# Kernel optimization log

Hardware: AMD Instinct MI355X
Metric: run time of the kernel (lower is better)

Reference implementation:

```python
import jax, jax.numpy as jnp
import numpy as np

N = 100000      # nodes
F_IN = 500      # num_features
H = 128         # num_hidden
C = 40          # num_classes
E = 3200000     # structural edges
K = 5           # knn neighbors


def setup_inputs() -> dict:
    key = jax.random.key(0)
    ks = jax.random.split(key, 9)
    x = jax.random.normal(ks[0], (N, F_IN), dtype=jnp.float32)
    edge_index = jax.random.randint(ks[1], (2, E), 0, N, dtype=jnp.int64)
    # knn graph: source i repeated K times, targets random (stand-in for cosine-KNN)
    src = jnp.repeat(jnp.arange(N, dtype=jnp.int64), K)
    dst = jax.random.randint(ks[2], (K * N,), 0, N, dtype=jnp.int64)
    edge_index_knn = jnp.stack([src, dst])
    s = lambda f: np.float32(1.0 / np.sqrt(f))
    W1 = jax.random.normal(ks[3], (F_IN, H), jnp.float32) * s(F_IN)
    b1 = jnp.zeros((H,), jnp.float32)
    W2 = jax.random.normal(ks[4], (2 * H, C), jnp.float32) * s(2 * H)
    b2 = jnp.zeros((C,), jnp.float32)
    Wlin = jax.random.normal(ks[5], (C, 2 * C), jnp.float32) * s(2 * C)  # torch Linear layout [out,in]
    blin = jnp.zeros((C,), jnp.float32)
    return {"x": x, "edge_index": edge_index, "edge_index_knn": edge_index_knn,
            "W1": W1, "b1": b1, "W2": W2, "b2": b2, "Wlin": Wlin, "blin": blin}


def gcn_conv(x, W, b, edge_index):
    # PyG GCNConv: add self-loops, symmetric normalization deg^-1/2 A deg^-1/2, x@W, scatter-add, +bias
    n = x.shape[0]
    loop = jnp.arange(n, dtype=edge_index.dtype)
    row = jnp.concatenate([edge_index[0], loop])  # sources (gathered)
    col = jnp.concatenate([edge_index[1], loop])  # targets (scattered)
    deg = jax.ops.segment_sum(jnp.ones_like(col, x.dtype), col, num_segments=n)
    dinv = jnp.where(deg > 0, jax.lax.rsqrt(jnp.maximum(deg, 1e-12)), 0.0).astype(x.dtype)
    norm = dinv[row] * dinv[col]                      # [E+n]
    h = x @ W                                          # [n, out]
    agg = jax.ops.segment_sum(h[row] * norm[:, None], col, num_segments=n)
    return agg + b


def reference(x, edge_index, edge_index_knn, W1, b1, W2, b2, Wlin, blin):
    h1 = gcn_conv(x, W1, b1, edge_index)
    h1_2 = gcn_conv(x, W1, b1, edge_index_knn)
    R1 = jax.nn.relu(jnp.concatenate([h1, h1_2], axis=1))  # dropout identity (eval mode)
    h2 = gcn_conv(R1, W2, b2, edge_index)
    h2_2 = gcn_conv(R1, W2, b2, edge_index_knn)
    R2 = jnp.concatenate([h2, h2_2], axis=1)
    logits = R2 @ Wlin.T + blin
    return jax.nn.log_softmax(logits, axis=1)
```

## Files before the change

kernel.cpp:

```cpp
#include <hip/hip_runtime.h>
#include <stdint.h>

#define NN   100000
#define FIN  500
#define HID  128
#define KP1  512
#define K2   256
#define CO   40
#define NPQ  80
#define NBUCK 391
#define CAPB_S 9216
#define CAPB_K 1536

typedef __attribute__((ext_vector_type(8))) short short8;
typedef __attribute__((ext_vector_type(4))) float float4v;
typedef __attribute__((address_space(3))) unsigned int as3_u32;
typedef __attribute__((address_space(1))) unsigned int as1_u32;

__device__ __forceinline__ unsigned short f2bf(float f) {
  unsigned u = __float_as_uint(f);
  u = u + 0x7fffu + ((u >> 16) & 1u);
  return (unsigned short)(u >> 16);
}
__device__ __forceinline__ float bf2f(unsigned short s) {
  return __uint_as_float(((unsigned)s) << 16);
}
__device__ __forceinline__ void gl_lds16(const void* g, void* l) {
  __builtin_amdgcn_global_load_lds((const as1_u32*)g, (as3_u32*)l, 16, 0, 0);
}

__global__ __launch_bounds__(256) void k_bin(
    const int* __restrict__ ei, int nS, int nb1S, int* __restrict__ gcur_s, int* __restrict__ gbin_s,
    const int* __restrict__ eik, int nK, int* __restrict__ gcur_k, int* __restrict__ gbin_k) {
  __shared__ int cnt[NBUCK];
  __shared__ int base[NBUCK];
  const int b = blockIdx.x;
  const bool knn = (b >= nb1S);
  const int* src = knn ? eik      : ei;
  const int* tgt = knn ? eik + nK : ei + nS;
  const int n    = knn ? nK : nS;
  int* gcur      = knn ? gcur_k : gcur_s;
  int* gbin      = knn ? gbin_k : gbin_s;
  const int capb = knn ? CAPB_K : CAPB_S;
  const int ebase = (knn ? b - nb1S : b) * 4096;
  const int t = threadIdx.x;

  for (int i = t; i < NBUCK; i += 256) cnt[i] = 0;
  __syncthreads();
  int s[16], g[16];
#pragma unroll
  for (int i = 0; i < 16; ++i) {
    const int e = ebase + i * 256 + t;
    const bool v = e < n;
    s[i] = v ? src[e] : 0;
    g[i] = v ? tgt[e] : -1;
    if (v) atomicAdd(&cnt[g[i] >> 8], 1);
  }
  __syncthreads();
  for (int i = t; i < NBUCK; i += 256) {
    const int c = cnt[i];
    base[i] = c ? atomicAdd(&gcur[i], c) : 0;
    cnt[i] = 0;
  }
  __syncthreads();
#pragma unroll
  for (int i = 0; i < 16; ++i) {
    if (g[i] >= 0) {
      const int bkt = g[i] >> 8;
      const int pos = base[bkt] + atomicAdd(&cnt[bkt], 1);
      if (pos < capb) gbin[bkt * capb + pos] = (s[i] << 8) | (g[i] & 255);
    }
  }
}

__global__ __launch_bounds__(512) void k_bscan(const int* __restrict__ gcur_s, int* __restrict__ bscan_s,
                                               const int* __restrict__ gcur_k, int* __restrict__ bscan_k) {
  __shared__ int sd[512];
  const int* gcur = blockIdx.x ? gcur_k : gcur_s;
  int* bscan      = blockIdx.x ? bscan_k : bscan_s;
  const int t = threadIdx.x;
  const int v = (t < NBUCK) ? gcur[t] : 0;
  sd[t] = v;
  __syncthreads();
  for (int off = 1; off < 512; off <<= 1) {
    const int x = (t >= off) ? sd[t - off] : 0;
    __syncthreads(); sd[t] += x; __syncthreads();
  }
  if (t < NBUCK) bscan[t] = sd[t] - v;
}

__global__ __launch_bounds__(256) void k_csr(
    const int* __restrict__ gcur_s, const int* __restrict__ gbin_s, const int* __restrict__ bscan_s,
    int* __restrict__ rp_s, int2* __restrict__ colw_s, float* __restrict__ dinv_s,
    const int* __restrict__ gcur_k, const int* __restrict__ gbin_k, const int* __restrict__ bscan_k,
    int* __restrict__ rp_k, int2* __restrict__ colw_k, float* __restrict__ dinv_k) {
  __shared__ int cnt[256];
  __shared__ int base[256];
  const int b0 = blockIdx.x;
  const bool knn = (b0 >= NBUCK);
  const int b = knn ? b0 - NBUCK : b0;
  const int* gcur  = knn ? gcur_k  : gcur_s;
  const int* gbin  = knn ? gbin_k  : gbin_s;
  const int* bscan = knn ? bscan_k : bscan_s;
  int* rp     = knn ? rp_k   : rp_s;
  int2* colw  = knn ? colw_k : colw_s;
  float* dinv = knn ? dinv_k : dinv_s;
  const int capb = knn ? CAPB_K : CAPB_S;
  const int t = threadIdx.x;
  int nB = gcur[b]; if (nB > capb) nB = capb;
  const int gb0 = b * capb;
  const int gbase = bscan[b];

  cnt[t] = 0;
  __syncthreads();
  for (int i = t; i < nB; i += 256) atomicAdd(&cnt[gbin[gb0 + i] & 255], 1);
  __syncthreads();
  const int myc = cnt[t];
  base[t] = myc;
  __syncthreads();
  for (int off = 1; off < 256; off <<= 1) {
    const int x = (t >= off) ? base[t - off] : 0;
    __syncthreads(); base[t] += x; __syncthreads();
  }
  const int excl = base[t] - myc;
  const int tg = b * 256 + t;
  if (tg < NN) { rp[tg] = gbase + excl; dinv[tg] = rsqrtf((float)(myc + 1)); }
  if (tg == NN) rp[NN] = gbase + excl;
  __syncthreads();
  base[t] = excl; cnt[t] = 0;
  __syncthreads();
  for (int i = t; i < nB; i += 256) {
    const int e = gbin[gb0 + i];
    const int tl = e & 255;
    const int pos = atomicAdd(&cnt[tl], 1);
    colw[gbase + base[tl] + pos] = make_int2(e >> 8, 0);
  }
}

__global__ __launch_bounds__(256) void k_fuse(
    int2* __restrict__ colw_s, const float* __restrict__ dinv_s, int nS, int nbF,
    int2* __restrict__ colw_k, const float* __restrict__ dinv_k, int nK) {
  const int b = blockIdx.x;
  if (b < nbF) {
    const int i = b * 256 + threadIdx.x;
    if (i < nS) {
      const int s = colw_s[i].x;
      colw_s[i].y = __float_as_int(dinv_s[s]);
    }
  } else {
    const int i = (b - nbF) * 256 + threadIdx.x;
    if (i < nK) {
      const int s = colw_k[i].x;
      colw_k[i].y = __float_as_int(dinv_k[s]);
    }
  }
}

__global__ void k_w1t(const float* __restrict__ W1, unsigned short* __restrict__ W1T) {
  int idx = blockIdx.x * 256 + threadIdx.x;
  int n = idx >> 9, k = idx & 511;
  float v = (k < FIN) ? W1[k * HID + n] : 0.f;
  W1T[idx] = f2bf(v);
}
__global__ void k_wpq(const float* __restrict__ W2, const float* __restrict__ Wl,
                      const float* __restrict__ b2, const float* __restrict__ bl,
                      unsigned short* __restrict__ WpqT, float* __restrict__ cb) {
  const int idx = blockIdx.x * 256 + threadIdx.x;
  const int n = idx >> 8, k = idx & 255;
  const int o = (n < CO) ? n : n - CO;
  const int joff = (n < CO) ? 0 : CO;
  float s = 0.f;
#pragma unroll 8
  for (int j = 0; j < CO; ++j) s += W2[k * CO + j] * Wl[o * NPQ + joff + j];
  WpqT[n * K2 + k] = f2bf(s);
  if (blockIdx.x == 0 && threadIdx.x < CO) {
    const int oo = threadIdx.x;
    float c = bl[oo];
    for (int j = 0; j < CO; ++j) c += b2[j] * (Wl[oo * NPQ + j] + Wl[oo * NPQ + CO + j]);
    cb[oo] = c;
  }
}

__global__ __launch_bounds__(256) void k_gemm1(const float* __restrict__ x,
    const unsigned short* __restrict__ W1T, const float* __restrict__ zbuf,
    unsigned short* __restrict__ H1b) {
  __shared__ float Als[2][512 * 4];
  __shared__ unsigned short Bls[2][512 * 8];
  const int t = threadIdx.x;
  const int wv = t >> 6, lane = t & 63;
  const int qd = lane >> 4, mr = lane & 15;
  const int m0 = blockIdx.x * 64;

  float4v acc[8];
  const float4v zf4 = {0.f, 0.f, 0.f, 0.f};
#pragma unroll
  for (int b = 0; b < 8; ++b) acc[b] = zf4;

  auto stage = [&](int kk, int pb) {
    const int k0 = kk * 32;
#pragma unroll
    for (int i = 0; i < 2; ++i) {
      const int cb = i * 256 + wv * 64;
      const int q = cb + lane;
      const int kg = q >> 6, m = q & 63;
      const int gm = m0 + m, kb = k0 + kg * 4;
      const float* gp = (gm < NN && kb < FIN) ? (x + (size_t)gm * FIN + kb) : zbuf;
      gl_lds16(gp, &Als[pb][cb * 4]);
    }
#pragma unroll
    for (int i = 0; i < 2; ++i) {
      const int cb = i * 256 + wv * 64;
      const int q = cb + lane;
      const int kg = q >> 7, n = q & 127;
      gl_lds16(W1T + n * KP1 + k0 + kg * 8, &Bls[pb][cb * 8]);
    }
  };

  stage(0, 0);
  for (int kk = 0; kk < 16; ++kk) {
    const int cur = kk & 1;
    if (kk + 1 < 16) {
      stage(kk + 1, cur ^ 1);
      asm volatile("s_waitcnt vmcnt(4)" ::: "memory");
    } else {
      asm volatile("s_waitcnt vmcnt(0)" ::: "memory");
    }
    __builtin_amdgcn_s_barrier();

    short8 af;
    {
      const int m = wv * 16 + mr;
      const float4v a0 = *(const float4v*)&Als[cur][((2 * qd) * 64 + m) * 4];
      const float4v a1 = *(const float4v*)&Als[cur][((2 * qd + 1) * 64 + m) * 4];
      af[0] = (short)f2bf(a0[0]); af[1] = (short)f2bf(a0[1]);
      af[2] = (short)f2bf(a0[2]); af[3] = (short)f2bf(a0[3]);
      af[4] = (short)f2bf(a1[0]); af[5] = (short)f2bf(a1[1]);
      af[6] = (short)f2bf(a1[2]); af[7] = (short)f2bf(a1[3]);
    }
#pragma unroll
    for (int ct = 0; ct < 8; ++ct) {
      const short8 bf = *(const short8*)&Bls[cur][(qd * 128 + ct * 16 + mr) * 8];
      acc[ct] = __builtin_amdgcn_mfma_f32_16x16x32_bf16(af, bf, acc[ct], 0, 0, 0);
    }
    __builtin_amdgcn_s_barrier();
  }

  const int rb = m0 + wv * 16 + qd * 4;
#pragma unroll
  for (int ct = 0; ct < 8; ++ct) {
    const int col = ct * 16 + mr;
#pragma unroll
    for (int j = 0; j < 4; ++j) {
      const int r = rb + j;
      if (r < NN) H1b[(size_t)r * HID + col] = f2bf(acc[ct][j]);
    }
  }
}

__global__ __launch_bounds__(256) void k_gemm2(const unsigned short* __restrict__ R1b,
    const unsigned short* __restrict__ WpqT, const unsigned short* __restrict__ zbuf,
    unsigned short* __restrict__ PQ) {
  __shared__ unsigned short Als[512 * 8];
  __shared__ unsigned short Bls[320 * 8];
  const int t = threadIdx.x;
  const int wv = t >> 6, lane = t & 63;
  const int qd = lane >> 4, mr = lane & 15;
  const int m0 = blockIdx.x * 128;

  float4v acc[2][5];
  const float4v zf4 = {0.f, 0.f, 0.f, 0.f};
#pragma unroll
  for (int a = 0; a < 2; ++a)
#pragma unroll
    for (int b = 0; b < 5; ++b) acc[a][b] = zf4;

  for (int kk = 0; kk < 8; ++kk) {
    const int k0 = kk * 32;
    __syncthreads();
#pragma unroll
    for (int i = 0; i < 2; ++i) {
      const int cb = (wv * 2 + i) * 64;
      const int q = cb + lane;
      const int kg = q >> 7, m = q & 127;
      const int gm = m0 + m;
      const unsigned short* gp = (gm < NN) ? (R1b + (size_t)gm * K2 + k0 + kg * 8) : zbuf;
      gl_lds16(gp, &Als[cb * 8]);
    }
    {
      const int cb = wv * 64;
      const int q = cb + lane;
      const int kg = q / 80, n = q % 80;
      gl_lds16(WpqT + n * K2 + k0 + kg * 8, &Bls[cb * 8]);
      if (wv == 0) {
        const int cb2 = 4 * 64;
        const int q2 = cb2 + lane;
        const int kg2 = q2 / 80, n2 = q2 % 80;
        gl_lds16(WpqT + n2 * K2 + k0 + kg2 * 8, &Bls[cb2 * 8]);
      }
    }
    __syncthreads();
    short8 af[2];
#pragma unroll
    for (int rt = 0; rt < 2; ++rt)
      af[rt] = *(const short8*)&Als[(qd * 128 + wv * 32 + rt * 16 + mr) * 8];
#pragma unroll
    for (int ct = 0; ct < 5; ++ct) {
      const short8 bf = *(const short8*)&Bls[(qd * 80 + ct * 16 + mr) * 8];
      acc[0][ct] = __builtin_amdgcn_mfma_f32_16x16x32_bf16(af[0], bf, acc[0][ct], 0, 0, 0);
      acc[1][ct] = __builtin_amdgcn_mfma_f32_16x16x32_bf16(af[1], bf, acc[1][ct], 0, 0, 0);
    }
  }
#pragma unroll
  for (int rt = 0; rt < 2; ++rt) {
    const int rb = m0 + wv * 32 + rt * 16 + qd * 4;
#pragma unroll
    for (int ct = 0; ct < 5; ++ct) {
      const int col = ct * 16 + mr;
#pragma unroll
      for (int j = 0; j < 4; ++j) {
        const int r = rb + j;
        if (r < NN) PQ[(size_t)r * NPQ + col] = f2bf(acc[rt][ct][j]);
      }
    }
  }
}

__device__ __forceinline__ void ld8(const int2* __restrict__ cw, int base, int e1, bool full,
                                    int2* __restrict__ q) {
  if (full) {
#pragma unroll
    for (int j = 0; j < 8; ++j) q[j] = cw[base + j];
  } else {
    const int e1c = e1 - 1;
#pragma unroll
    for (int j = 0; j < 8; ++j) {
      const int ee = base + j;
      int2 t = cw[(ee < e1) ? ee : e1c];
      t.y = (ee < e1) ? t.y : 0;
      q[j] = t;
    }
  }
}
__device__ __forceinline__ void g8(const int2* __restrict__ q,
    const unsigned* __restrict__ H32, int lane, unsigned* __restrict__ d) {
#pragma unroll
  for (int j = 0; j < 8; ++j) d[j] = H32[(size_t)q[j].x * 64 + lane];
}
__device__ __forceinline__ void f8(const int2* __restrict__ q, const unsigned* __restrict__ d,
                                   float& ax, float& ay) {
#pragma unroll
  for (int j = 0; j < 8; ++j) {
    const float w = __int_as_float(q[j].y);
    ax += w * __uint_as_float(d[j] << 16);
    ay += w * __uint_as_float(d[j] & 0xffff0000u);
  }
}

__global__ __launch_bounds__(256) void k_agg1(
    const int* __restrict__ rp_s, const int2* __restrict__ colw_s, const float* __restrict__ dinv_s,
    const int* __restrict__ rp_k, const int2* __restrict__ colw_k, const float* __restrict__ dinv_k,
    const unsigned short* __restrict__ H, const float* __restrict__ bias,
    unsigned short* __restrict__ out) {
  const int wv = threadIdx.x >> 6, lane = threadIdx.x & 63;
  const int c = blockIdx.x * 4 + wv;
  if (c >= NN) return;
  const unsigned* H32 = (const unsigned*)H;
  const int e0s = __builtin_amdgcn_readfirstlane(rp_s[c]);
  const int e1s = __builtin_amdgcn_readfirstlane(rp_s[c + 1]);
  const int e0k = __builtin_amdgcn_readfirstlane(rp_k[c]);
  const int e1k = __builtin_amdgcn_readfirstlane(rp_k[c + 1]);
  const int nbS = (e1s - e0s + 7) >> 3;
  const int nbK = (e1k - e0k + 7) >> 3;

  int2 q0[8], q1[8], qk[8];
  unsigned d0[8], d1[8], dk[8];
  const unsigned pc = H32[(size_t)c * 64 + lane];
  if (nbS > 0) { ld8(colw_s, e0s, e1s, e0s + 8 <= e1s, q0); g8(q0, H32, lane, d0); }
  if (nbS > 1) { ld8(colw_s, e0s + 8, e1s, e0s + 16 <= e1s, q1); g8(q1, H32, lane, d1); }
  if (nbK > 0) { ld8(colw_k, e0k, e1k, e0k + 8 <= e1k, qk); g8(qk, H32, lane, dk); }

  const float dcs = dinv_s[c], dck = dinv_k[c];
  const float slo = __uint_as_float(pc << 16);
  const float shi = __uint_as_float(pc & 0xffff0000u);
  float ax = dcs * slo, ay = dcs * shi;
  float bx = dck * slo, by = dck * shi;

  int b = 0;
  while (b + 2 < nbS) {
    f8(q0, d0, ax, ay);
    {
      const int bs = e0s + (b + 2) * 8;
      ld8(colw_s, bs, e1s, bs + 8 <= e1s, q0);
      g8(q0, H32, lane, d0);
    }
    f8(q1, d1, ax, ay);
    if (b + 3 < nbS) {
      const int bs = e0s + (b + 3) * 8;
      ld8(colw_s, bs, e1s, bs + 8 <= e1s, q1);
      g8(q1, H32, lane, d1);
    }
    b += 2;
  }
  if (b < nbS) f8(q0, d0, ax, ay);
  if (b + 1 < nbS) f8(q1, d1, ax, ay);

  if (nbK > 0) f8(qk, dk, bx, by);
  for (int bk = 1; bk < nbK; ++bk) {
    const int bs = e0k + bk * 8;
    ld8(colw_k, bs, e1k, bs + 8 <= e1k, qk);
    g8(qk, H32, lane, dk);
    f8(qk, dk, bx, by);
  }

  const float2 bb = ((const float2*)bias)[lane];
  const float o0 = fmaxf(dcs * ax + bb.x, 0.f);
  const float o1 = fmaxf(dcs * ay + bb.y, 0.f);
  const float o2 = fmaxf(dck * bx + bb.x, 0.f);
  const float o3 = fmaxf(dck * by + bb.y, 0.f);
  unsigned* orow = (unsigned*)(out + (size_t)c * K2);
  orow[lane]      = (unsigned)f2bf(o0) | ((unsigned)f2bf(o1) << 16);
  orow[64 + lane] = (unsigned)f2bf(o2) | ((unsigned)f2bf(o3) << 16);
}

__global__ __launch_bounds__(256) void k_aggf(
    const int* __restrict__ rp_s, const int2* __restrict__ colw_s, const float* __restrict__ dinv_s,
    const int* __restrict__ rp_k, const int2* __restrict__ colw_k, const float* __restrict__ dinv_k,
    const unsigned short* __restrict__ PQ, const float* __restrict__ cb,
    float* __restrict__ out) {
  const int wv = threadIdx.x >> 6, lane = threadIdx.x & 63;
  const int c = blockIdx.x * 4 + wv;
  if (c >= NN) return;
  const unsigned* PQ32 = (const unsigned*)PQ;
  const int g = lane / 20;
  const int l = lane % 20;
  float sx = 0.f, sy = 0.f, kx = 0.f, ky = 0.f;
  if (g < 3) {
    {
      const int e1 = rp_s[c + 1];
      int e = rp_s[c] + g;
      for (; e + 9 < e1; e += 12) {
        const int2 q0 = colw_s[e], q1 = colw_s[e + 3], q2 = colw_s[e + 6], q3 = colw_s[e + 9];
        const unsigned d0 = PQ32[(size_t)q0.x * 40 + l];
        const unsigned d1 = PQ32[(size_t)q1.x * 40 + l];
        const unsigned d2 = PQ32[(size_t)q2.x * 40 + l];
        const unsigned d3 = PQ32[(size_t)q3.x * 40 + l];
        const float w0 = __int_as_float(q0.y), w1 = __int_as_float(q1.y);
        const float w2 = __int_as_float(q2.y), w3 = __int_as_float(q3.y);
        sx += w0 * __uint_as_float(d0 << 16) + w1 * __uint_as_float(d1 << 16)
            + w2 * __uint_as_float(d2 << 16) + w3 * __uint_as_float(d3 << 16);
        sy += w0 * __uint_as_float(d0 & 0xffff0000u) + w1 * __uint_as_float(d1 & 0xffff0000u)
            + w2 * __uint_as_float(d2 & 0xffff0000u) + w3 * __uint_as_float(d3 & 0xffff0000u);
      }
      for (; e < e1; e += 3) {
        const int2 q = colw_s[e];
        const unsigned d = PQ32[(size_t)q.x * 40 + l];
        const float w = __int_as_float(q.y);
        sx += w * __uint_as_float(d << 16);
        sy += w * __uint_as_float(d & 0xffff0000u);
      }
    }
    {
      const int e1 = rp_k[c + 1];
      int e = rp_k[c] + g;
      for (; e < e1; e += 3) {
        const int2 q = colw_k[e];
        const unsigned d = PQ32[(size_t)q.x * 40 + 20 + l];
        const float w = __int_as_float(q.y);
        kx += w * __uint_as_float(d << 16);
        ky += w * __uint_as_float(d & 0xffff0000u);
      }
    }
  }
  sx += __shfl(sx, lane + 20) + __shfl(sx, lane + 40);
  sy += __shfl(sy, lane + 20) + __shfl(sy, lane + 40);
  kx += __shfl(kx, lane + 20) + __shfl(kx, lane + 40);
  ky += __shfl(ky, lane + 20) + __shfl(ky, lane + 40);

  float lo = 0.f, hi = 0.f;
  if (lane < 20) {
    const float dcs = dinv_s[c], dck = dinv_k[c];
    const unsigned dP = PQ32[(size_t)c * 40 + lane];
    const unsigned dQ = PQ32[(size_t)c * 40 + 20 + lane];
    const float2 cbb = ((const float2*)cb)[lane];
    lo = dcs * (sx + dcs * __uint_as_float(dP << 16))
       + dck * (kx + dck * __uint_as_float(dQ << 16)) + cbb.x;
    hi = dcs * (sy + dcs * __uint_as_float(dP & 0xffff0000u))
       + dck * (ky + dck * __uint_as_float(dQ & 0xffff0000u)) + cbb.y;
  }
  float m = (lane < 20) ? fmaxf(lo, hi) : -3.4e38f;
#pragma unroll
  for (int off = 1; off < 64; off <<= 1) m = fmaxf(m, __shfl_xor(m, off));
  float s = (lane < 20) ? (expf(lo - m) + expf(hi - m)) : 0.f;
#pragma unroll
  for (int off = 1; off < 64; off <<= 1) s += __shfl_xor(s, off);
  const float lse = m + logf(s);
  if (lane < 20) {
    float2 o; o.x = lo - lse; o.y = hi - lse;
    ((float2*)(out + (size_t)c * CO))[lane] = o;
  }
}

extern "C" void kernel_launch(void* const* d_in, const int* in_sizes, int n_in,
                              void* d_out, int out_size, void* d_ws, size_t ws_size,
                              hipStream_t stream) {
  const float* x  = (const float*)d_in[0];
  const int* ei   = (const int*)d_in[1];
  const int* eik  = (const int*)d_in[2];
  const float* W1 = (const float*)d_in[3];
  const float* b1 = (const float*)d_in[4];
  const float* W2 = (const float*)d_in[5];
  const float* b2 = (const float*)d_in[6];
  const float* Wl = (const float*)d_in[7];
  const float* bl = (const float*)d_in[8];
  float* out = (float*)d_out;
  const int E  = in_sizes[1] / 2;
  const int EK = in_sizes[2] / 2;

  char* p = (char*)d_ws;
  size_t off = 0;
  auto alloc = [&](size_t bytes) -> void* {
    void* r = (void*)(p + off);
    off += (bytes + 255) & ~(size_t)255;
    return r;
  };
  int* gcur_s = (int*)alloc((size_t)NBUCK * 4);
  int* gcur_k = (int*)alloc((size_t)NBUCK * 4);
  void* zbuf = alloc(256);
  const size_t zero_span = off;
  int* bscan_s = (int*)alloc((size_t)NBUCK * 4);
  int* bscan_k = (int*)alloc((size_t)NBUCK * 4);
  float* dinv_s = (float*)alloc((size_t)NN * 4);
  float* dinv_k = (float*)alloc((size_t)NN * 4);
  int* rp_s = (int*)alloc((size_t)(NN + 1) * 4);
  int* rp_k = (int*)alloc((size_t)(NN + 1) * 4);
  unsigned short* W1T = (unsigned short*)alloc((size_t)HID * KP1 * 2);
  unsigned short* WpqT = (unsigned short*)alloc((size_t)NPQ * K2 * 2);
  float* cbv = (float*)alloc((size_t)CO * 4);
  int* gbin_s = (int*)alloc((size_t)NBUCK * CAPB_S * 4);
  int* gbin_k = (int*)alloc((size_t)NBUCK * CAPB_K * 4);
  int2* colw_s = (int2*)alloc((size_t)E * 8);
  int2* colw_k = (int2*)alloc((size_t)EK * 8);
  unsigned short* H1b = (unsigned short*)alloc((size_t)NN * HID * 2);
  unsigned short* R1b = (unsigned short*)alloc((size_t)NN * K2 * 2);
  unsigned short* PQ = H1b;

  hipMemsetAsync(d_ws, 0, zero_span, stream);

  const int nb1S = (E + 4095) / 4096;
  const int nb1K = (EK + 4095) / 4096;
  k_bin<<<nb1S + nb1K, 256, 0, stream>>>(ei, E, nb1S, gcur_s, gbin_s, eik, EK, gcur_k, gbin_k);
  k_bscan<<<2, 512, 0, stream>>>(gcur_s, bscan_s, gcur_k, bscan_k);
  k_csr<<<2 * NBUCK, 256, 0, stream>>>(gcur_s, gbin_s, bscan_s, rp_s, colw_s, dinv_s,
                                       gcur_k, gbin_k, bscan_k, rp_k, colw_k, dinv_k);
  const int nbF = (E + 255) / 256;
  const int nbFk = (EK + 255) / 256;
  k_fuse<<<nbF + nbFk, 256, 0, stream>>>(colw_s, dinv_s, E, nbF, colw_k, dinv_k, EK);

  k_w1t<<<(HID * KP1) / 256, 256, 0, stream>>>(W1, W1T);
  k_wpq<<<NPQ, 256, 0, stream>>>(W2, Wl, b2, bl, WpqT, cbv);

  k_gemm1<<<(NN + 63) / 64, 256, 0, stream>>>(x, W1T, (const float*)zbuf, H1b);
  const int nbAgg = (NN + 3) / 4;
  k_agg1<<<nbAgg, 256, 0, stream>>>(rp_s, colw_s, dinv_s, rp_k, colw_k, dinv_k, H1b, b1, R1b);

  k_gemm2<<<(NN + 127) / 128, 256, 0, stream>>>(R1b, WpqT, (const unsigned short*)zbuf, PQ);
  k_aggf<<<nbAgg, 256, 0, stream>>>(rp_s, colw_s, dinv_s, rp_k, colw_k, dinv_k, PQ, cbv, out);
}
```

Baseline: 714.2 us.

## Swizzle LDS layouts in both GEMMs and double-buffer gemm2 with smaller tiles

```diff
diff --git a/kernel.cpp b/kernel.cpp
--- a/kernel.cpp
+++ b/kernel.cpp
@@ -8,6 +8,7 @@
 #define K2   256
 #define CO   40
 #define NPQ  80
+#define NPQP 128
 #define NBUCK 391
 #define CAPB_S 9216
 #define CAPB_K 1536
@@ -200,19 +201,19 @@
     const int k0 = kk * 32;
 #pragma unroll
     for (int i = 0; i < 2; ++i) {
-      const int cb = i * 256 + wv * 64;
-      const int q = cb + lane;
-      const int kg = q >> 6, m = q & 63;
+      const int q = (wv * 2 + i) * 64 + lane;
+      const int m = q >> 3;
+      const int kg = (q & 7) ^ (m & 7);
       const int gm = m0 + m, kb = k0 + kg * 4;
       const float* gp = (gm < NN && kb < FIN) ? (x + (size_t)gm * FIN + kb) : zbuf;
-      gl_lds16(gp, &Als[pb][cb * 4]);
+      gl_lds16(gp, &Als[pb][q * 4]);
     }
 #pragma unroll
     for (int i = 0; i < 2; ++i) {
-      const int cb = i * 256 + wv * 64;
-      const int q = cb + lane;
-      const int kg = q >> 7, n = q & 127;
-      gl_lds16(W1T + n * KP1 + k0 + kg * 8, &Bls[pb][cb * 8]);
+      const int q = (wv * 2 + i) * 64 + lane;
+      const int n = q >> 2;
+      const int kg = (q & 3) ^ ((q >> 3) & 3);
+      gl_lds16(W1T + n * KP1 + k0 + kg * 8, &Bls[pb][q * 8]);
     }
   };
 
@@ -230,8 +231,10 @@
     short8 af;
     {
       const int m = wv * 16 + mr;
-      const float4v a0 = *(const float4v*)&Als[cur][((2 * qd) * 64 + m) * 4];
-      const float4v a1 = *(const float4v*)&Als[cur][((2 * qd + 1) * 64 + m) * 4];
+      const int s0 = m * 8 + ((2 * qd) ^ (m & 7));
+      const int s1 = m * 8 + ((2 * qd + 1) ^ (m & 7));
+      const float4v a0 = *(const float4v*)&Als[cur][s0 * 4];
+      const float4v a1 = *(const float4v*)&Als[cur][s1 * 4];
       af[0] = (short)f2bf(a0[0]); af[1] = (short)f2bf(a0[1]);
       af[2] = (short)f2bf(a0[2]); af[3] = (short)f2bf(a0[3]);
       af[4] = (short)f2bf(a1[0]); af[5] = (short)f2bf(a1[1]);
@@ -239,7 +242,9 @@
     }
 #pragma unroll
     for (int ct = 0; ct < 8; ++ct) {
-      const short8 bf = *(const short8*)&Bls[cur][(qd * 128 + ct * 16 + mr) * 8];
+      const int n = ct * 16 + mr;
+      const int sb = n * 4 + (qd ^ ((n >> 1) & 3));
+      const short8 bf = *(const short8*)&Bls[cur][sb * 8];
       acc[ct] = __builtin_amdgcn_mfma_f32_16x16x32_bf16(af, bf, acc[ct], 0, 0, 0);
     }
     __builtin_amdgcn_s_barrier();
@@ -260,67 +265,72 @@
 __global__ __launch_bounds__(256) void k_gemm2(const unsigned short* __restrict__ R1b,
     const unsigned short* __restrict__ WpqT, const unsigned short* __restrict__ zbuf,
     unsigned short* __restrict__ PQ) {
-  __shared__ unsigned short Als[512 * 8];
-  __shared__ unsigned short Bls[320 * 8];
+  __shared__ unsigned short Als[2][256 * 8];
+  __shared__ unsigned short Bls[2][512 * 8];
   const int t = threadIdx.x;
   const int wv = t >> 6, lane = t & 63;
   const int qd = lane >> 4, mr = lane & 15;
-  const int m0 = blockIdx.x * 128;
-
-  float4v acc[2][5];
+  const int m0 = blockIdx.x * 64;
+
+  float4v acc[5];
   const float4v zf4 = {0.f, 0.f, 0.f, 0.f};
 #pragma unroll
-  for (int a = 0; a < 2; ++a)
-#pragma unroll
-    for (int b = 0; b < 5; ++b) acc[a][b] = zf4;
-
-  for (int kk = 0; kk < 8; ++kk) {
+  for (int b = 0; b < 5; ++b) acc[b] = zf4;
+
+  auto stage = [&](int kk, int pb) {
     const int k0 = kk * 32;
-    __syncthreads();
-#pragma unroll
-    for (int i = 0; i < 2; ++i) {
-      const int cb = (wv * 2 + i) * 64;
-      const int q = cb + lane;
-      const int kg = q >> 7, m = q & 127;
+    {
+      const int q = wv * 64 + lane;
+      const int m = q >> 2;
+      const int kg = (q & 3) ^ ((q >> 3) & 3);
       const int gm = m0 + m;
       const unsigned short* gp = (gm < NN) ? (R1b + (size_t)gm * K2 + k0 + kg * 8) : zbuf;
-      gl_lds16(gp, &Als[cb * 8]);
-    }
+      gl_lds16(gp, &Als[pb][q * 8]);
+    }
+#pragma unroll
+    for (int i = 0; i < 2; ++i) {
+      const int q = (wv * 2 + i) * 64 + lane;
+      const int n = q >> 2;
+      const int kg = (q & 3) ^ ((q >> 3) & 3);
+      gl_lds16(WpqT + n * K2 + k0 + kg * 8, &Bls[pb][q * 8]);
+    }
+  };
+
+  stage(0, 0);
+  for (int kk = 0; kk < 8; ++kk) {
+    const int cur = kk & 1;
+    if (kk + 1 < 8) {
+      stage(kk + 1, cur ^ 1);
+      asm volatile("s_waitcnt vmcnt(3)" ::: "memory");
+    } else {
+      asm volatile("s_waitcnt vmcnt(0)" ::: "memory");
+    }
+    __builtin_amdgcn_s_barrier();
+
+    short8 af;
     {
-      const int cb = wv * 64;
-      const int q = cb + lane;
-      const int kg = q / 80, n = q % 80;
-      gl_lds16(WpqT + n * K2 + k0 + kg * 8, &Bls[cb * 8]);
-      if (wv == 0) {
-        const int cb2 = 4 * 64;
-        const int q2 = cb2 + lane;
-        const int kg2 = q2 / 80, n2 = q2 % 80;
-        gl_lds16(WpqT + n2 * K2 + k0 + kg2 * 8, &Bls[cb2 * 8]);
-      }
-    }
-    __syncthreads();
-    short8 af[2];
-#pragma unroll
-    for (int rt = 0; rt < 2; ++rt)
-      af[rt] = *(const short8*)&Als[(qd * 128 + wv * 32 + rt * 16 + mr) * 8];
+      const int m = wv * 16 + mr;
+      const int sa = m * 4 + (qd ^ ((m >> 1) & 3));
+      af = *(const short8*)&Als[cur][sa * 8];
+    }
 #pragma unroll
     for (int ct = 0; ct < 5; ++ct) {
-      const short8 bf = *(const short8*)&Bls[(qd * 80 + ct * 16 + mr) * 8];
-      acc[0][ct] = __builtin_amdgcn_mfma_f32_16x16x32_bf16(af[0], bf, acc[0][ct], 0, 0, 0);
-      acc[1][ct] = __builtin_amdgcn_mfma_f32_16x16x32_bf16(af[1], bf, acc[1][ct], 0, 0, 0);
-    }
-  }
-#pragma unroll
-  for (int rt = 0; rt < 2; ++rt) {
-    const int rb = m0 + wv * 32 + rt * 16 + qd * 4;
-#pragma unroll
-    for (int ct = 0; ct < 5; ++ct) {
-      const int col = ct * 16 + mr;
-#pragma unroll
-      for (int j = 0; j < 4; ++j) {
-        const int r = rb + j;
-        if (r < NN) PQ[(size_t)r * NPQ + col] = f2bf(acc[rt][ct][j]);
-      }
+      const int n = ct * 16 + mr;
+      const int sb = n * 4 + (qd ^ ((n >> 1) & 3));
+      const short8 bf = *(const short8*)&Bls[cur][sb * 8];
+      acc[ct] = __builtin_amdgcn_mfma_f32_16x16x32_bf16(af, bf, acc[ct], 0, 0, 0);
+    }
+    __builtin_amdgcn_s_barrier();
+  }
+
+  const int rb = m0 + wv * 16 + qd * 4;
+#pragma unroll
+  for (int ct = 0; ct < 5; ++ct) {
+    const int col = ct * 16 + mr;
+#pragma unroll
+    for (int j = 0; j < 4; ++j) {
+      const int r = rb + j;
+      if (r < NN) PQ[(size_t)r * NPQ + col] = f2bf(acc[ct][j]);
     }
   }
 }
@@ -534,7 +544,7 @@
   int* rp_s = (int*)alloc((size_t)(NN + 1) * 4);
   int* rp_k = (int*)alloc((size_t)(NN + 1) * 4);
   unsigned short* W1T = (unsigned short*)alloc((size_t)HID * KP1 * 2);
-  unsigned short* WpqT = (unsigned short*)alloc((size_t)NPQ * K2 * 2);
+  unsigned short* WpqT = (unsigned short*)alloc((size_t)NPQP * K2 * 2);
   float* cbv = (float*)alloc((size_t)CO * 4);
   int* gbin_s = (int*)alloc((size_t)NBUCK * CAPB_S * 4);
   int* gbin_k = (int*)alloc((size_t)NBUCK * CAPB_K * 4);
@@ -563,6 +573,6 @@
   const int nbAgg = (NN + 3) / 4;
   k_agg1<<<nbAgg, 256, 0, stream>>>(rp_s, colw_s, dinv_s, rp_k, colw_k, dinv_k, H1b, b1, R1b);
 
-  k_gemm2<<<(NN + 127) / 128, 256, 0, stream>>>(R1b, WpqT, (const unsigned short*)zbuf, PQ);
+  k_gemm2<<<(NN + 63) / 64, 256, 0, stream>>>(R1b, WpqT, (const unsigned short*)zbuf, PQ);
   k_aggf<<<nbAgg, 256, 0, stream>>>(rp_s, colw_s, dinv_s, rp_k, colw_k, dinv_k, PQ, cbv, out);
 }
```

Result: faster. 688.8 us (-3.6%).
